# Kernel optimization log

Hardware: AMD Instinct MI355X
Metric: run time of the kernel (lower is better)

Reference implementation:

```python
import jax, jax.numpy as jnp
import numpy as np

NEG_SLOPE = 0.01  # torch F.leaky_relu default


def _gat_stack(x, W, a1w, a1b, a2w, a2b):
    """One GAT stack over all heads.
    x: (B, N, F_in); W: (H, F_in, d); a1w/a2w: (H, d); a1b/a2b: (H,)
    returns (B, N, H*d) -- heads concatenated in order along last dim.
    """
    # 1x1 conv1d (no bias) == per-node linear projection
    fts = jnp.einsum('bnf,hfd->hbnd', x, W)                      # (H,B,N,d)
    f1 = jnp.einsum('hbnd,hd->hbn', fts, a1w) + a1b[:, None, None]
    f2 = jnp.einsum('hbnd,hd->hbn', fts, a2w) + a2b[:, None, None]
    # logits[h,b,i,j] = f1[h,b,i] + f2[h,b,j]  (f_1.permute + f_2 broadcast)
    logits = f1[:, :, :, None] + f2[:, :, None, :]               # (H,B,N,N)
    coefs = jax.nn.softmax(jax.nn.leaky_relu(logits, NEG_SLOPE), axis=-1)
    vals = jnp.einsum('hbnm,hbmd->hbnd', coefs, fts)             # bmm aggregation
    ret = jax.nn.elu(vals + fts)                                 # residual-within-head + ELU activation
    B, N = x.shape[0], x.shape[1]
    return jnp.transpose(ret, (1, 2, 0, 3)).reshape(B, N, -1)    # cat(heads, dim=-1)


def setup_inputs() -> dict:
    key = jax.random.key(0)
    ks = jax.random.split(key, 7)
    B, N, F_in, H, d = 32, 512, 128, 8, 64
    hidden = H * d  # 512
    s = 0.05
    return {
        'x':   jax.random.normal(ks[0], (B, N, F_in), jnp.float32),
        'W0':  jax.random.normal(ks[1], (H, F_in, d), jnp.float32) * s,
        'W1':  jax.random.normal(ks[2], (H, hidden, d), jnp.float32) * s,
        'a1w': jax.random.normal(ks[3], (2, H, d), jnp.float32) * s,
        'a1b': jax.random.normal(ks[4], (2, H), jnp.float32) * s,
        'a2w': jax.random.normal(ks[5], (2, H, d), jnp.float32) * s,
        'a2b': jax.random.normal(ks[6], (2, H), jnp.float32) * s,
    }


def reference(x, W0, W1, a1w, a1b, a2w, a2b):
    # stack 0: input dim = num_random_sample
    h = _gat_stack(x, W0, a1w[0], a1b[0], a2w[0], a2b[0])
    # stack 1: input dim = hidden_dim
    out = _gat_stack(h, W1, a1w[1], a1b[1], a2w[1], a2b[1])
    return out
```

## Files before the change

kernel.cpp:

```cpp
#include <hip/hip_runtime.h>
#include <hip/hip_bf16.h>
#include <stdint.h>

typedef __attribute__((ext_vector_type(8))) short short8;
typedef __attribute__((ext_vector_type(4))) float f32x4;

#define L2E 1.44269504f
#define FN  131072

__device__ __forceinline__ short f2bf(float f) {
    unsigned u = __builtin_bit_cast(unsigned, f);
    return (short)((u + 0x8000u) >> 16);
}
__device__ __forceinline__ float bf2f(short s) {
    unsigned u = ((unsigned)(unsigned short)s) << 16;
    return __builtin_bit_cast(float, u);
}

__device__ __forceinline__ void gld16(void* l, const void* g) {
    __builtin_amdgcn_global_load_lds(
        (const __attribute__((address_space(1))) unsigned*)g,
        (__attribute__((address_space(3))) unsigned*)l, 16, 0, 0);
}

__global__ void wtrans_kernel(const float* __restrict__ W0, const float* __restrict__ W1,
                              short* __restrict__ BT0, short* __restrict__ BT1) {
    int idx = blockIdx.x * 256 + threadIdx.x;
    if (idx < 8 * 128 * 64) {
        int h = idx >> 13;
        int k = (idx >> 6) & 127;
        int dd = idx & 63;
        BT0[(h * 64 + dd) * 128 + k] = f2bf(W0[idx]);
    } else {
        int j = idx - 8 * 128 * 64;
        int h = j >> 15;
        int k = (j >> 6) & 511;
        int dd = j & 63;
        BT1[(h * 64 + dd) * 512 + k] = f2bf(W1[j]);
    }
}

template <typename AT>
__global__ __launch_bounds__(256, 2)
void gemm_kernel(const AT* __restrict__ A, const short* __restrict__ BT,
                 short* __restrict__ fts, int K,
                 const float* __restrict__ a1w, const float* __restrict__ a1b,
                 const float* __restrict__ a2w, const float* __restrict__ a2b,
                 float* __restrict__ fbuf) {
    __shared__ __align__(16) short As[128 * 64];
    __shared__ __align__(16) short Bs[128 * 64];

    const int tid  = threadIdx.x;
    const int lane = tid & 63;
    const int w    = tid >> 6;
    const int wr   = w >> 1, wc = w & 1;
    const int quad = lane >> 4, l15 = lane & 15;
    const int m0   = blockIdx.y * 128;
    const int n0   = blockIdx.x * 128;

    const int rl   = lane >> 3;
    const int cpos = lane & 7;
    const int kcl  = cpos ^ rl;

    f32x4 acc[4][4];
    for (int i = 0; i < 4; ++i)
        for (int j = 0; j < 4; ++j) { f32x4 z = {0.f, 0.f, 0.f, 0.f}; acc[i][j] = z; }

    const int nkb = K >> 6;
    for (int kb = 0; kb < nkb; ++kb) {
        __syncthreads();
        if constexpr (sizeof(AT) == 4) {
            for (int i = 0; i < 8; ++i) {
                int id  = tid + i * 256;
                int row = id >> 4, q = id & 15;
                int c = q >> 1, half = q & 1;
                float4 v = *(const float4*)((const float*)A + (size_t)(m0 + row) * K + kb * 64 + q * 4);
                ushort4 p;
                p.x = (unsigned short)f2bf(v.x);
                p.y = (unsigned short)f2bf(v.y);
                p.z = (unsigned short)f2bf(v.z);
                p.w = (unsigned short)f2bf(v.w);
                int swz = c ^ (row & 7);
                *(ushort4*)(As + row * 64 + swz * 8 + half * 4) = p;
            }
        } else {
            for (int i = 0; i < 4; ++i) {
                int rowb = w * 32 + i * 8;
                gld16(As + rowb * 64,
                      (const short*)A + (size_t)(m0 + rowb + rl) * K + kb * 64 + kcl * 8);
            }
        }
        for (int i = 0; i < 4; ++i) {
            int rowb = w * 32 + i * 8;
            gld16(Bs + rowb * 64,
                  BT + (size_t)(n0 + rowb + rl) * K + kb * 64 + kcl * 8);
        }
        __syncthreads();
        short8 af[2][4], bf[2][4];
        for (int ks = 0; ks < 2; ++ks) {
            for (int mf = 0; mf < 4; ++mf) {
                int row = wr * 64 + mf * 16 + l15;
                af[ks][mf] = *(const short8*)(As + row * 64 + (((ks * 4 + quad) ^ (row & 7)) << 3));
            }
            for (int nf = 0; nf < 4; ++nf) {
                int row = wc * 64 + nf * 16 + l15;
                bf[ks][nf] = *(const short8*)(Bs + row * 64 + (((ks * 4 + quad) ^ (row & 7)) << 3));
            }
        }
        for (int ks = 0; ks < 2; ++ks)
            for (int mf = 0; mf < 4; ++mf)
                for (int nf = 0; nf < 4; ++nf)
                    acc[mf][nf] = __builtin_amdgcn_mfma_f32_16x16x32_bf16(af[ks][mf], bf[ks][nf], acc[mf][nf], 0, 0, 0);
    }

    for (int nf = 0; nf < 4; ++nf) {
        int col = n0 + wc * 64 + nf * 16 + l15;
        int h = col >> 6, dd = col & 63;
        for (int mf = 0; mf < 4; ++mf) {
            int m = m0 + wr * 64 + mf * 16 + quad * 4;
            int b = m >> 9, n = m & 511;
            ushort4 pk;
            pk.x = (unsigned short)f2bf(acc[mf][nf][0]);
            pk.y = (unsigned short)f2bf(acc[mf][nf][1]);
            pk.z = (unsigned short)f2bf(acc[mf][nf][2]);
            pk.w = (unsigned short)f2bf(acc[mf][nf][3]);
            *(ushort4*)(fts + (size_t)((h * 32 + b) * 64 + dd) * 512 + n) = pk;
        }
    }

    {
        const int head = (n0 >> 6) + wc;
        float w1[4], w2[4];
        for (int nf = 0; nf < 4; ++nf) {
            w1[nf] = a1w[head * 64 + nf * 16 + l15];
            w2[nf] = a2w[head * 64 + nf * 16 + l15];
        }
        const float b1 = a1b[head], b2 = a2b[head];
        const int rsel = l15 & 3;
        for (int mf = 0; mf < 4; ++mf) {
            float g1[4], g2[4];
            for (int r = 0; r < 4; ++r) {
                float s1 = 0.f, s2 = 0.f;
                for (int nf = 0; nf < 4; ++nf) {
                    s1 += acc[mf][nf][r] * w1[nf];
                    s2 += acc[mf][nf][r] * w2[nf];
                }
                for (int m = 1; m < 16; m <<= 1) {
                    s1 += __shfl_xor(s1, m, 64);
                    s2 += __shfl_xor(s2, m, 64);
                }
                g1[r] = s1; g2[r] = s2;
            }
            float v1 = rsel == 0 ? g1[0] : rsel == 1 ? g1[1] : rsel == 2 ? g1[2] : g1[3];
            float v2 = rsel == 0 ? g2[0] : rsel == 1 ? g2[1] : rsel == 2 ? g2[2] : g2[3];
            if (l15 < 4) {
                int m = m0 + wr * 64 + mf * 16 + quad * 4 + rsel;
                int b = m >> 9, i = m & 511;
                int fi = (head * 32 + b) * 512 + i;
                float f1 = v1 + b1, f2 = v2 + b2;
                fbuf[0 * FN + fi] = __builtin_amdgcn_exp2f(f1 * L2E);
                fbuf[1 * FN + fi] = __builtin_amdgcn_exp2f(f1 * (0.01f * L2E));
                fbuf[2 * FN + fi] = __builtin_amdgcn_exp2f(f2 * L2E);
                fbuf[3 * FN + fi] = __builtin_amdgcn_exp2f(f2 * (0.01f * L2E));
            }
        }
    }
}

template <typename OutT>
__global__ __launch_bounds__(256, 4)
void attn_kernel(const short* __restrict__ fts, const float* __restrict__ fbuf,
                 OutT* __restrict__ out) {
    __shared__ __align__(16) short fts_s[64 * 256];
    __shared__ __align__(16) float p2_s[256];
    __shared__ __align__(16) float q2_s[256];

    const int tid  = threadIdx.x;
    const int lane = tid & 63, w = tid >> 6;
    const int quad = lane >> 4, l15 = lane & 15;
    const int bx   = blockIdx.x;
    const int h    = bx >> 7;
    const int b    = (bx >> 2) & 31;
    const int quarter = bx & 3;
    const int r0   = quarter * 128;
    const size_t fbase = (size_t)((h * 32 + b) * 64) * 512;
    const int fidx = (h * 32 + b) * 512;

    f32x4 acc[2][4], accL[2];
    for (int i = 0; i < 2; ++i) {
        f32x4 z = {0.f, 0.f, 0.f, 0.f};
        accL[i] = z;
        for (int j = 0; j < 4; ++j) acc[i][j] = z;
    }
    short8 onesv;
    for (int t = 0; t < 8; ++t) onesv[t] = (short)0x3F80;

    float P1r[2], Q1r[2];
    for (int rt = 0; rt < 2; ++rt) {
        int i = fidx + r0 + w * 32 + rt * 16 + l15;
        P1r[rt] = fbuf[i];
        Q1r[rt] = fbuf[1 * FN + i];
    }

    for (int c = 0; c < 2; ++c) {
        __syncthreads();
        for (int i = 0; i < 8; ++i) {
            int id = tid + i * 256;
            int dd = id >> 5, nc = id & 31;
            gld16(fts_s + (i * 256 + w * 64) * 8,
                  fts + fbase + dd * 512 + c * 256 + ((nc ^ (dd & 7)) << 3));
        }
        {
            int j = fidx + c * 256 + tid;
            p2_s[tid] = fbuf[2 * FN + j];
            q2_s[tid] = fbuf[3 * FN + j];
        }
        __syncthreads();

        for (int jb = 0; jb < 8; ++jb) {
            short8 bfr[4];
            for (int nf = 0; nf < 4; ++nf) {
                int col = nf * 16 + l15;
                bfr[nf] = *(const short8*)(fts_s + col * 256 + (((jb * 4 + quad) ^ (col & 7)) << 3));
            }
            int o = jb * 32 + quad * 8;
            f32x4 pa = *(const f32x4*)(p2_s + o), pb = *(const f32x4*)(p2_s + o + 4);
            f32x4 qa = *(const f32x4*)(q2_s + o), qb = *(const f32x4*)(q2_s + o + 4);
            float p2v[8] = {pa[0], pa[1], pa[2], pa[3], pb[0], pb[1], pb[2], pb[3]};
            float q2v[8] = {qa[0], qa[1], qa[2], qa[3], qb[0], qb[1], qb[2], qb[3]};

            for (int rt = 0; rt < 2; ++rt) {
                short8 ef;
                for (int t = 0; t < 8; ++t)
                    ef[t] = f2bf(fmaxf(P1r[rt] * p2v[t], Q1r[rt] * q2v[t]));
                for (int nf = 0; nf < 4; ++nf)
                    acc[rt][nf] = __builtin_amdgcn_mfma_f32_16x16x32_bf16(ef, bfr[nf], acc[rt][nf], 0, 0, 0);
                accL[rt] = __builtin_amdgcn_mfma_f32_16x16x32_bf16(ef, onesv, accL[rt], 0, 0, 0);
            }
        }
    }

    for (int rt = 0; rt < 2; ++rt) {
        float rinv[4];
        for (int r = 0; r < 4; ++r) rinv[r] = __builtin_amdgcn_rcpf(accL[rt][r]);
        int i0 = r0 + w * 32 + rt * 16 + quad * 4;
        for (int nf = 0; nf < 4; ++nf) {
            int col = nf * 16 + l15;
            ushort4 res = *(const ushort4*)(fts + fbase + col * 512 + i0);
            unsigned short rr[4] = {res.x, res.y, res.z, res.w};
            for (int r = 0; r < 4; ++r) {
                float val = acc[rt][nf][r] * rinv[r] + bf2f((short)rr[r]);
                if (val < 0.f) val = __builtin_amdgcn_exp2f(val * L2E) - 1.f;
                size_t oidx = (size_t)(b * 512 + i0 + r) * 512 + h * 64 + col;
                if constexpr (sizeof(OutT) == 4) out[oidx] = val;
                else                             out[oidx] = f2bf(val);
            }
        }
    }
}

extern "C" void kernel_launch(void* const* d_in, const int* in_sizes, int n_in,
                              void* d_out, int out_size, void* d_ws, size_t ws_size,
                              hipStream_t stream) {
    const float* x   = (const float*)d_in[0];
    const float* W0  = (const float*)d_in[1];
    const float* W1  = (const float*)d_in[2];
    const float* a1w = (const float*)d_in[3];
    const float* a1b = (const float*)d_in[4];
    const float* a2w = (const float*)d_in[5];
    const float* a2b = (const float*)d_in[6];
    float* out = (float*)d_out;

    char* ws = (char*)d_ws;
    short* BT0  = (short*)(ws);
    short* BT1  = (short*)(ws + 131072);
    float* fbuf = (float*)(ws + 655360);
    short* fts  = (short*)(ws + 2752512);
    short* hbuf = (short*)d_out;

    wtrans_kernel<<<1280, 256, 0, stream>>>(W0, W1, BT0, BT1);

    gemm_kernel<float><<<dim3(4, 128), 256, 0, stream>>>(x, BT0, fts, 128,
                                                         a1w, a1b, a2w, a2b, fbuf);
    attn_kernel<short><<<1024, 256, 0, stream>>>(fts, fbuf, hbuf);

    gemm_kernel<short><<<dim3(4, 128), 256, 0, stream>>>(hbuf, BT1, fts, 512,
                                                         a1w + 512, a1b + 8, a2w + 512, a2b + 8, fbuf);
    attn_kernel<float><<<1024, 256, 0, stream>>>(fts, fbuf, out);
}
```

Before: 160.7 us.

## Read attention operands directly from global memory instead of staging in LDS

Removes the LDS staging of fts tiles and p2/q2 vectors in the attention kernel, so each wave loads its MFMA B-fragments and softmax factors straight from global memory. It also reorders the block index so the four row-quarters of the same (head, batch) slab are spread across the grid. The aim is to drop the two __syncthreads per chunk and raise occupancy by freeing LDS. The cost is redundant global/L2 traffic, because all four waves reload the same fragments, and loss of the swizzled LDS layout.

Result: slower. 199.5 us (+24.2%).

```diff
diff --git a/kernel.cpp b/kernel.cpp
--- a/kernel.cpp
+++ b/kernel.cpp
@@ -171,20 +171,17 @@
 __global__ __launch_bounds__(256, 4)
 void attn_kernel(const short* __restrict__ fts, const float* __restrict__ fbuf,
                  OutT* __restrict__ out) {
-    __shared__ __align__(16) short fts_s[64 * 256];
-    __shared__ __align__(16) float p2_s[256];
-    __shared__ __align__(16) float q2_s[256];
-
     const int tid  = threadIdx.x;
     const int lane = tid & 63, w = tid >> 6;
     const int quad = lane >> 4, l15 = lane & 15;
     const int bx   = blockIdx.x;
-    const int h    = bx >> 7;
-    const int b    = (bx >> 2) & 31;
-    const int quarter = bx & 3;
+    const int quarter = bx >> 8;
+    const int slab = bx & 255;
+    const int h    = slab >> 5;
+    const int b    = slab & 31;
     const int r0   = quarter * 128;
-    const size_t fbase = (size_t)((h * 32 + b) * 64) * 512;
-    const int fidx = (h * 32 + b) * 512;
+    const size_t fbase = (size_t)(slab * 64) * 512;
+    const int fidx = slab * 512;
 
     f32x4 acc[2][4], accL[2];
     for (int i = 0; i < 2; ++i) {
@@ -202,30 +199,21 @@
         Q1r[rt] = fbuf[1 * FN + i];
     }
 
+    const float* p2g = fbuf + 2 * FN + fidx;
+    const float* q2g = fbuf + 3 * FN + fidx;
+
+#pragma unroll
     for (int c = 0; c < 2; ++c) {
-        __syncthreads();
-        for (int i = 0; i < 8; ++i) {
-            int id = tid + i * 256;
-            int dd = id >> 5, nc = id & 31;
-            gld16(fts_s + (i * 256 + w * 64) * 8,
-                  fts + fbase + dd * 512 + c * 256 + ((nc ^ (dd & 7)) << 3));
-        }
-        {
-            int j = fidx + c * 256 + tid;
-            p2_s[tid] = fbuf[2 * FN + j];
-            q2_s[tid] = fbuf[3 * FN + j];
-        }
-        __syncthreads();
-
+#pragma unroll
         for (int jb = 0; jb < 8; ++jb) {
+            const int kchunk = c * 256 + jb * 32 + quad * 8;
             short8 bfr[4];
             for (int nf = 0; nf < 4; ++nf) {
                 int col = nf * 16 + l15;
-                bfr[nf] = *(const short8*)(fts_s + col * 256 + (((jb * 4 + quad) ^ (col & 7)) << 3));
-            }
-            int o = jb * 32 + quad * 8;
-            f32x4 pa = *(const f32x4*)(p2_s + o), pb = *(const f32x4*)(p2_s + o + 4);
-            f32x4 qa = *(const f32x4*)(q2_s + o), qb = *(const f32x4*)(q2_s + o + 4);
+                bfr[nf] = *(const short8*)(fts + fbase + (size_t)col * 512 + kchunk);
+            }
+            f32x4 pa = *(const f32x4*)(p2g + kchunk), pb = *(const f32x4*)(p2g + kchunk + 4);
+            f32x4 qa = *(const f32x4*)(q2g + kchunk), qb = *(const f32x4*)(q2g + kchunk + 4);
             float p2v[8] = {pa[0], pa[1], pa[2], pa[3], pb[0], pb[1], pb[2], pb[3]};
             float q2v[8] = {qa[0], qa[1], qa[2], qa[3], qb[0], qb[1], qb[2], qb[3]};
 
```
